# Kernel optimization log

Measured on AMD Instinct MI355X. Metric: run time of the kernel, lower is better.

## Reference

```python
import jax, jax.numpy as jnp
import numpy as np

UP = 2


def _lpf_rect(N, cutoff):
    # ideal lowpass rect over full-FFT frequency axis (with Nyquist 0.5 fix)
    cutoff_low = int((N * cutoff) // 2)
    cutoff_high = int(N - cutoff_low)
    rect = np.ones(N, dtype=np.float32)
    rect[cutoff_low + 1:cutoff_high] = 0.0
    if (N * cutoff) % 2 == 0:
        rect[cutoff_low] = 0.5
        rect[cutoff_high] = 0.5
    return rect


def _recon_rect(N, cutoff):
    # reconstruction rect for zero-insertion upsampling (no Nyquist halving)
    cutoff_low = int((N * cutoff) // 2)
    cutoff_high = int(N - cutoff_low)
    rect = np.ones(N, dtype=np.float32)
    rect[cutoff_low + 1:cutoff_high] = 0.0
    return rect


def _rfft2_mask(rect_h, rect_w):
    # outer product mask on rfft2 grid: full H axis x half W axis
    half_w = rect_w.shape[0] // 2 + 1
    return jnp.asarray(rect_h[:, None] * rect_w[None, :half_w])


def setup_inputs() -> dict:
    key = jax.random.key(0)
    x = jax.random.normal(key, (32, 128, 64, 64), dtype=jnp.float32)
    # PolyAct default init_coef (buffer, non-trainable)
    coef = jnp.array([0.0169394634313126, 0.5, 0.3078363963999393, 0.0],
                     dtype=jnp.float32)
    return {"x": x, "coef": coef}


def reference(x, coef):
    B, C, H, W = x.shape
    Hu, Wu = H * UP, W * UP

    # ---- UpsampleRFFT: zero-insertion then ideal reconstruction filter ----
    xu = jnp.zeros((B, C, Hu, Wu), x.dtype).at[:, :, ::UP, ::UP].set(x)
    recon_mask = _rfft2_mask(_recon_rect(Hu, 1.0 / UP), _recon_rect(Wu, 1.0 / UP))
    f = jnp.fft.rfft2(xu) * (UP * UP) * recon_mask
    xu = jnp.fft.irfft2(f, s=(Hu, Wu))

    # ---- PolyAct: calc_polynomial loops range(2, deg) with deg=3, so only
    # terms up to x^2 are used (coef[3] is never applied) ----
    y = coef[0] + coef[1] * xu + coef[2] * xu * xu

    # ---- LPF_RFFT with cutoff = 1/up ----
    lpf_mask = _rfft2_mask(_lpf_rect(Hu, 1.0 / UP), _lpf_rect(Wu, 1.0 / UP))
    y = jnp.fft.irfft2(jnp.fft.rfft2(y) * lpf_mask, s=(Hu, Wu))

    # ---- decimate back to original resolution ----
    return y[:, :, ::UP, ::UP]
```

## Files before the change

### kernel.cpp

```cpp
#include <hip/hip_runtime.h>
#include <math.h>


typedef short short8 __attribute__((ext_vector_type(8)));
typedef float f32x16 __attribute__((ext_vector_type(16)));

#define LSH 68

__device__ unsigned g_flag;
__device__ float g_gws[64];
__device__ __align__(16) short g_ftw[16 * 64 * 8];

__device__ __forceinline__ short f2bf(float f) {
  unsigned u = __float_as_uint(f);
  u += 0x7FFFu + ((u >> 16) & 1u);
  return (short)(u >> 16);
}
__device__ __forceinline__ float bf2f(short s) {
  return __uint_as_float(((unsigned)(unsigned short)s) << 16);
}
__device__ __forceinline__ short8 ldrow(const short* p) {
  union { unsigned u[4]; short8 s; } v;
  const uint2 lo = *(const uint2*)p;
  const uint2 hi = *(const uint2*)(p + 4);
  v.u[0] = lo.x; v.u[1] = lo.y; v.u[2] = hi.x; v.u[3] = hi.y;
  return v.s;
}
__device__ __forceinline__ unsigned pk2(short a, short b) {
  return (unsigned)(unsigned short)a | ((unsigned)(unsigned short)b << 16);
}

__global__ void uppolyact_setup() {
  if (g_flag == 0xC0FFEEu) return;
  __shared__ float g64s[64];
  const int tid = threadIdx.x;
  if (tid < 64) {
    const int d = 2 * tid + 1;
    float s = 1.0f;
    for (int k = 1; k <= 32; ++k) {
      const int qq = (k * d) & 127;
      s += 2.0f * cosf((float)M_PI * (1.0f / 64.0f) * (float)qq);
    }
    const float gv = s * (1.0f / 64.0f);
    g64s[tid] = gv;
    g_gws[tid] = gv;
  }
  __syncthreads();
#pragma unroll
  for (int e = 0; e < 4; ++e) {
    const int entry = tid + 256 * e;
    const int s_ = entry >> 6, ln = entry & 63;
    const int t_ = s_ >> 3, blk = (s_ >> 2) & 1, kk = s_ & 3;
    const int basei = kk * 16 + (ln >> 5) * 8 - (ln & 31) - 32 * blk;
    short* dst = &g_ftw[(s_ * 64 + ln) * 8];
#pragma unroll
    for (int j = 0; j < 8; ++j) {
      const int i0 = basei + j;
      const int idx = t_ ? ((-i0) & 63) : (i0 & 63);
      dst[j] = f2bf(g64s[idx]);
    }
  }
  __syncthreads();
  if (tid == 0) g_flag = 0xC0FFEEu;
}

__global__ __launch_bounds__(256, 4) void uppolyact_kernel(
    const float* __restrict__ x, const float* __restrict__ coef,
    float* __restrict__ out) {
  __shared__ __align__(16) short Xr[64 * LSH];
  __shared__ __align__(16) short XcZ[64 * LSH];
  __shared__ __align__(16) short LrU[64 * LSH];
  __shared__ __align__(16) short Zoo[64 * LSH];
  __shared__ float g64[64];
  __shared__ float tvec[64], uvec[64], sRv[64], Luv[64];
  __shared__ float sigv;

  const int tid = threadIdx.x;
  const int lane = tid & 63;
  const int w = tid >> 6;
  const int q = lane >> 5;
  const int l31 = lane & 31;
  const int rb = w >> 1, cb = w & 1;
  const int jcol = cb * 32 + l31;
  const size_t base = (size_t)blockIdx.x * 4096;
  const float* xb = x + base;
  const short8* ft8 = (const short8*)g_ftw;

  float xcur[16];
#pragma unroll
  for (int r = 0; r < 16; ++r) {
    const int irow = rb * 32 + (r & 3) + 4 * q + 8 * (r >> 2);
    xcur[r] = xb[irow * 64 + jcol];
  }

  short8 fA[4], fB[4];
#pragma unroll
  for (int kk = 0; kk < 4; ++kk) {
    fA[kk] = ft8[((2 + rb) * 4 + kk) * 64 + lane];
    fB[kk] = ft8[((2 + cb) * 4 + kk) * 64 + lane];
  }
  if (tid < 64) g64[tid] = g_gws[tid];

#pragma unroll
  for (int k = 0; k < 4; ++k) {
    const int irowb = rb * 32 + 4 * q + 8 * k;
    short b[4];
#pragma unroll
    for (int j = 0; j < 4; ++j) {
      b[j] = f2bf(xcur[4 * k + j]);
      Xr[(irowb + j) * LSH + jcol] = b[j];
    }
    uint2 p;
    p.x = pk2(b[0], b[1]);
    p.y = pk2(b[2], b[3]);
    *(uint2*)&XcZ[jcol * LSH + irowb] = p;
  }
  __syncthreads();

  {
    const int o = tid >> 1, h = tid & 1;
    const short* src = (o < 64) ? &XcZ[o * LSH + 32 * h]
                                : &Xr[(o - 64) * LSH + 32 * h];
    float acc = 0.0f;
#pragma unroll
    for (int p = 0; p < 4; ++p) {
      const short8 v = ldrow(src + 8 * p);
#pragma unroll
      for (int j = 0; j < 8; ++j) {
        const float f = bf2f(v[j]);
        acc += (j & 1) ? -f : f;
      }
    }
    acc += __shfl_xor(acc, 1);
    if (h == 0) {
      if (o < 64) tvec[o] = acc; else uvec[o - 64] = acc;
    }
  }
  __syncthreads();

  f32x16 Rt, Lt;
#pragma unroll
  for (int r = 0; r < 16; ++r) { Rt[r] = 0.0f; Lt[r] = 0.0f; }
#pragma unroll
  for (int kk = 0; kk < 4; ++kk) {
    const short8 bR = ldrow(&Xr[(cb * 32 + l31) * LSH + kk * 16 + q * 8]);
    Rt = __builtin_amdgcn_mfma_f32_32x32x16_bf16(fA[kk], bR, Rt, 0, 0, 0);
    const short8 aL = ldrow(&XcZ[(rb * 32 + l31) * LSH + kk * 16 + q * 8]);
    Lt = __builtin_amdgcn_mfma_f32_32x32x16_bf16(aL, fB[kk], Lt, 0, 0, 0);
  }
  {
    const int o = tid >> 1, h = tid & 1;
    const int o63 = o & 63;
    const float* vsrc = (o < 64) ? tvec : uvec;
    float acc = 0.0f;
#pragma unroll
    for (int p = 0; p < 32; ++p) {
      const int m = 32 * h + p;
      acc += vsrc[m] * g64[(o63 - m) & 63];
    }
    acc += __shfl_xor(acc, 1);
    if (h == 0) {
      if (o < 64) sRv[o] = acc; else Luv[o - 64] = acc;
    }
  }
  if (w == 0) {
    float sv = (lane & 1) ? -tvec[lane] : tvec[lane];
#pragma unroll
    for (int d_ = 1; d_ < 64; d_ <<= 1) sv += __shfl_xor(sv, d_);
    if (lane == 0) sigv = sv;
  }
  __syncthreads();

  float zoe[16];
  {
    const int icol = cb * 32 + l31;
    const float sgi = (icol & 1) ? -1.0f : 1.0f;
#pragma unroll
    for (int k = 0; k < 4; ++k) {
      const int jb = rb * 32 + 4 * q + 8 * k;
      short ze[4], zl[4];
#pragma unroll
      for (int t = 0; t < 4; ++t) {
        const int r = 4 * k + t;
        const int jrow = jb + t;
        const float sgj = (jrow & 1) ? -1.0f : 1.0f;
        const float veo = Rt[r] + sgi * sRv[jrow] * (1.0f / 64.0f);
        ze[t] = f2bf(veo * veo);
        zl[t] = f2bf(Lt[r]);
        const float voe = Lt[r] + Luv[icol] * sgj * (1.0f / 64.0f);
        zoe[r] = voe * voe;
      }
      uint2 pz, pl;
      pz.x = pk2(ze[0], ze[1]); pz.y = pk2(ze[2], ze[3]);
      pl.x = pk2(zl[0], zl[1]); pl.y = pk2(zl[2], zl[3]);
      *(uint2*)&XcZ[icol * LSH + jb] = pz;
      *(uint2*)&LrU[icol * LSH + jb] = pl;
    }
  }
  __syncthreads();

  short8 fU[4], fW[4];
#pragma unroll
  for (int kk = 0; kk < 4; ++kk) {
    fU[kk] = ft8[((0 + rb) * 4 + kk) * 64 + lane];
    fW[kk] = ft8[((0 + cb) * 4 + kk) * 64 + lane];
  }
  f32x16 OOt;
#pragma unroll
  for (int r = 0; r < 16; ++r) OOt[r] = 0.0f;
#pragma unroll
  for (int kk = 0; kk < 4; ++kk) {
    const short8 b = ldrow(&LrU[(cb * 32 + l31) * LSH + kk * 16 + q * 8]);
    OOt = __builtin_amdgcn_mfma_f32_32x32x16_bf16(fA[kk], b, OOt, 0, 0, 0);
  }
  {
    const int icol = cb * 32 + l31;
#pragma unroll
    for (int k = 0; k < 4; ++k) {
      const int jb = rb * 32 + 4 * q + 8 * k;
      short zo[4];
#pragma unroll
      for (int t = 0; t < 4; ++t) {
        const int r = 4 * k + t;
        zo[t] = f2bf(OOt[r] * OOt[r]);
      }
      uint2 p;
      p.x = pk2(zo[0], zo[1]); p.y = pk2(zo[2], zo[3]);
      *(uint2*)&Zoo[icol * LSH + jb] = p;
    }
  }
  __syncthreads();

  f32x16 Ut, Wv;
#pragma unroll
  for (int r = 0; r < 16; ++r) { Ut[r] = zoe[r]; Wv[r] = 0.0f; }
#pragma unroll
  for (int kk = 0; kk < 4; ++kk) {
    const short8 bU = ldrow(&Zoo[(cb * 32 + l31) * LSH + kk * 16 + q * 8]);
    Ut = __builtin_amdgcn_mfma_f32_32x32x16_bf16(fU[kk], bU, Ut, 0, 0, 0);
    const short8 aW = ldrow(&XcZ[(rb * 32 + l31) * LSH + kk * 16 + q * 8]);
    Wv = __builtin_amdgcn_mfma_f32_32x32x16_bf16(aW, fW[kk], Wv, 0, 0, 0);
  }
#pragma unroll
  for (int r = 0; r < 16; ++r) {
    const int jrow = rb * 32 + (r & 3) + 4 * q + 8 * (r >> 2);
    const int icol = cb * 32 + l31;
    LrU[jrow * LSH + icol] = f2bf(Ut[r]);
  }
  __syncthreads();

  f32x16 Vv;
#pragma unroll
  for (int r = 0; r < 16; ++r) Vv[r] = 0.0f;
#pragma unroll
  for (int kk = 0; kk < 4; ++kk) {
    const short8 b = ldrow(&LrU[(cb * 32 + l31) * LSH + kk * 16 + q * 8]);
    Vv = __builtin_amdgcn_mfma_f32_32x32x16_bf16(fU[kk], b, Vv, 0, 0, 0);
  }

  const float c0 = coef[0], c1 = coef[1];
  const float c2q = 0.25f * coef[2];
  float* ob = out + base;
#pragma unroll
  for (int r = 0; r < 16; ++r) {
    const int irow = rb * 32 + (r & 3) + 4 * q + 8 * (r >> 2);
    const float sgi = (irow & 1) ? -1.0f : 1.0f;
    const float sgj = (jcol & 1) ? -1.0f : 1.0f;
    const float xv_ = bf2f(f2bf(xcur[r]));
    const float vee = xv_ + (sgi * tvec[jcol] + uvec[irow] * sgj) * (1.0f / 64.0f) +
                      sgi * sgj * sigv * (1.0f / 4096.0f);
    const float zee = vee * vee;
    ob[irow * 64 + jcol] = c0 + c1 * xcur[r] + c2q * (zee + Vv[r] + Wv[r]);
  }
}

extern "C" void kernel_launch(void* const* d_in, const int* in_sizes, int n_in,
                              void* d_out, int out_size, void* d_ws,
                              size_t ws_size, hipStream_t stream) {
  const float* x = (const float*)d_in[0];
  const float* coef = (const float*)d_in[1];
  float* out = (float*)d_out;
  const int channels = out_size / 4096;
  uppolyact_setup<<<dim3(1), dim3(256), 0, stream>>>();
  uppolyact_kernel<<<dim3(channels), dim3(256), 0, stream>>>(x, coef, out);
}
```

Before: 126.5 us.

## Stage Fourier twiddle fragments in LDS instead of holding them in registers

The bf16 twiddle MFMA operands were held in 16 short8 registers per thread, loaded from global memory. They now go cooperatively into a shared ftab array, refilled once between phases, and each MFMA reads its fragment from LDS. The shared buffers are also reordered so one 64x68 tile is freed to hold the table. This lowers VGPR pressure and global fragment traffic, at the cost of extra LDS reads per MFMA and one more barrier.

```diff
diff --git a/kernel.cpp b/kernel.cpp
--- a/kernel.cpp
+++ b/kernel.cpp
@@ -4,6 +4,7 @@
 
 typedef short short8 __attribute__((ext_vector_type(8)));
 typedef float f32x16 __attribute__((ext_vector_type(16)));
+typedef float f32x4 __attribute__((ext_vector_type(4)));
 
 #define LSH 68
 
@@ -67,10 +68,10 @@
 __global__ __launch_bounds__(256, 4) void uppolyact_kernel(
     const float* __restrict__ x, const float* __restrict__ coef,
     float* __restrict__ out) {
-  __shared__ __align__(16) short Xr[64 * LSH];
-  __shared__ __align__(16) short XcZ[64 * LSH];
-  __shared__ __align__(16) short LrU[64 * LSH];
-  __shared__ __align__(16) short Zoo[64 * LSH];
+  __shared__ __align__(16) short bufA[64 * LSH];
+  __shared__ __align__(16) short bufB[64 * LSH];
+  __shared__ __align__(16) short bufC[64 * LSH];
+  __shared__ __align__(16) short ftab[8 * 64 * 8];
   __shared__ float g64[64];
   __shared__ float tvec[64], uvec[64], sRv[64], Luv[64];
   __shared__ float sigv;
@@ -84,7 +85,6 @@
   const int jcol = cb * 32 + l31;
   const size_t base = (size_t)blockIdx.x * 4096;
   const float* xb = x + base;
-  const short8* ft8 = (const short8*)g_ftw;
 
   float xcur[16];
 #pragma unroll
@@ -92,12 +92,11 @@
     const int irow = rb * 32 + (r & 3) + 4 * q + 8 * (r >> 2);
     xcur[r] = xb[irow * 64 + jcol];
   }
-
-  short8 fA[4], fB[4];
-#pragma unroll
-  for (int kk = 0; kk < 4; ++kk) {
-    fA[kk] = ft8[((2 + rb) * 4 + kk) * 64 + lane];
-    fB[kk] = ft8[((2 + cb) * 4 + kk) * 64 + lane];
+  f32x4 t0, t1;
+  {
+    const f32x4* fsrc = (const f32x4*)(g_ftw + 8 * 64 * 8);
+    t0 = fsrc[tid];
+    t1 = fsrc[tid + 256];
   }
   if (tid < 64) g64[tid] = g_gws[tid];
 
@@ -108,19 +107,24 @@
 #pragma unroll
     for (int j = 0; j < 4; ++j) {
       b[j] = f2bf(xcur[4 * k + j]);
-      Xr[(irowb + j) * LSH + jcol] = b[j];
+      bufA[(irowb + j) * LSH + jcol] = b[j];
     }
     uint2 p;
     p.x = pk2(b[0], b[1]);
     p.y = pk2(b[2], b[3]);
-    *(uint2*)&XcZ[jcol * LSH + irowb] = p;
+    *(uint2*)&bufB[jcol * LSH + irowb] = p;
+  }
+  {
+    f32x4* fdst = (f32x4*)ftab;
+    fdst[tid] = t0;
+    fdst[tid + 256] = t1;
   }
   __syncthreads();
 
   {
     const int o = tid >> 1, h = tid & 1;
-    const short* src = (o < 64) ? &XcZ[o * LSH + 32 * h]
-                                : &Xr[(o - 64) * LSH + 32 * h];
+    const short* src = (o < 64) ? &bufB[o * LSH + 32 * h]
+                                : &bufA[(o - 64) * LSH + 32 * h];
     float acc = 0.0f;
 #pragma unroll
     for (int p = 0; p < 4; ++p) {
@@ -143,10 +147,12 @@
   for (int r = 0; r < 16; ++r) { Rt[r] = 0.0f; Lt[r] = 0.0f; }
 #pragma unroll
   for (int kk = 0; kk < 4; ++kk) {
-    const short8 bR = ldrow(&Xr[(cb * 32 + l31) * LSH + kk * 16 + q * 8]);
-    Rt = __builtin_amdgcn_mfma_f32_32x32x16_bf16(fA[kk], bR, Rt, 0, 0, 0);
-    const short8 aL = ldrow(&XcZ[(rb * 32 + l31) * LSH + kk * 16 + q * 8]);
-    Lt = __builtin_amdgcn_mfma_f32_32x32x16_bf16(aL, fB[kk], Lt, 0, 0, 0);
+    const short8 aR = *(const short8*)&ftab[((rb * 4 + kk) * 64 + lane) * 8];
+    const short8 bR = ldrow(&bufA[(cb * 32 + l31) * LSH + kk * 16 + q * 8]);
+    Rt = __builtin_amdgcn_mfma_f32_32x32x16_bf16(aR, bR, Rt, 0, 0, 0);
+    const short8 aL = ldrow(&bufB[(rb * 32 + l31) * LSH + kk * 16 + q * 8]);
+    const short8 bL = *(const short8*)&ftab[((cb * 4 + kk) * 64 + lane) * 8];
+    Lt = __builtin_amdgcn_mfma_f32_32x32x16_bf16(aL, bL, Lt, 0, 0, 0);
   }
   {
     const int o = tid >> 1, h = tid & 1;
@@ -171,6 +177,12 @@
   }
   __syncthreads();
 
+  f32x4 u0, u1;
+  {
+    const f32x4* fsrc = (const f32x4*)g_ftw;
+    u0 = fsrc[tid];
+    u1 = fsrc[tid + 256];
+  }
   float zoe[16];
   {
     const int icol = cb * 32 + l31;
@@ -193,25 +205,20 @@
       uint2 pz, pl;
       pz.x = pk2(ze[0], ze[1]); pz.y = pk2(ze[2], ze[3]);
       pl.x = pk2(zl[0], zl[1]); pl.y = pk2(zl[2], zl[3]);
-      *(uint2*)&XcZ[icol * LSH + jb] = pz;
-      *(uint2*)&LrU[icol * LSH + jb] = pl;
-    }
-  }
-  __syncthreads();
-
-  short8 fU[4], fW[4];
+      *(uint2*)&bufA[icol * LSH + jb] = pz;
+      *(uint2*)&bufB[icol * LSH + jb] = pl;
+    }
+  }
+  __syncthreads();
+
+  f32x16 OOt;
+#pragma unroll
+  for (int r = 0; r < 16; ++r) OOt[r] = 0.0f;
 #pragma unroll
   for (int kk = 0; kk < 4; ++kk) {
-    fU[kk] = ft8[((0 + rb) * 4 + kk) * 64 + lane];
-    fW[kk] = ft8[((0 + cb) * 4 + kk) * 64 + lane];
-  }
-  f32x16 OOt;
-#pragma unroll
-  for (int r = 0; r < 16; ++r) OOt[r] = 0.0f;
-#pragma unroll
-  for (int kk = 0; kk < 4; ++kk) {
-    const short8 b = ldrow(&LrU[(cb * 32 + l31) * LSH + kk * 16 + q * 8]);
-    OOt = __builtin_amdgcn_mfma_f32_32x32x16_bf16(fA[kk], b, OOt, 0, 0, 0);
+    const short8 a = *(const short8*)&ftab[((rb * 4 + kk) * 64 + lane) * 8];
+    const short8 b = ldrow(&bufB[(cb * 32 + l31) * LSH + kk * 16 + q * 8]);
+    OOt = __builtin_amdgcn_mfma_f32_32x32x16_bf16(a, b, OOt, 0, 0, 0);
   }
   {
     const int icol = cb * 32 + l31;
@@ -226,8 +233,16 @@
       }
       uint2 p;
       p.x = pk2(zo[0], zo[1]); p.y = pk2(zo[2], zo[3]);
-      *(uint2*)&Zoo[icol * LSH + jb] = p;
-    }
+      *(uint2*)&bufC[icol * LSH + jb] = p;
+    }
+  }
+  asm volatile("" : "+v"(u0), "+v"(u1));
+  __syncthreads();
+
+  {
+    f32x4* fdst = (f32x4*)ftab;
+    fdst[tid] = u0;
+    fdst[tid + 256] = u1;
   }
   __syncthreads();
 
@@ -236,16 +251,18 @@
   for (int r = 0; r < 16; ++r) { Ut[r] = zoe[r]; Wv[r] = 0.0f; }
 #pragma unroll
   for (int kk = 0; kk < 4; ++kk) {
-    const short8 bU = ldrow(&Zoo[(cb * 32 + l31) * LSH + kk * 16 + q * 8]);
-    Ut = __builtin_amdgcn_mfma_f32_32x32x16_bf16(fU[kk], bU, Ut, 0, 0, 0);
-    const short8 aW = ldrow(&XcZ[(rb * 32 + l31) * LSH + kk * 16 + q * 8]);
-    Wv = __builtin_amdgcn_mfma_f32_32x32x16_bf16(aW, fW[kk], Wv, 0, 0, 0);
+    const short8 aU = *(const short8*)&ftab[((rb * 4 + kk) * 64 + lane) * 8];
+    const short8 bU = ldrow(&bufC[(cb * 32 + l31) * LSH + kk * 16 + q * 8]);
+    Ut = __builtin_amdgcn_mfma_f32_32x32x16_bf16(aU, bU, Ut, 0, 0, 0);
+    const short8 aW = ldrow(&bufA[(rb * 32 + l31) * LSH + kk * 16 + q * 8]);
+    const short8 bW = *(const short8*)&ftab[((cb * 4 + kk) * 64 + lane) * 8];
+    Wv = __builtin_amdgcn_mfma_f32_32x32x16_bf16(aW, bW, Wv, 0, 0, 0);
   }
 #pragma unroll
   for (int r = 0; r < 16; ++r) {
     const int jrow = rb * 32 + (r & 3) + 4 * q + 8 * (r >> 2);
     const int icol = cb * 32 + l31;
-    LrU[jrow * LSH + icol] = f2bf(Ut[r]);
+    bufB[jrow * LSH + icol] = f2bf(Ut[r]);
   }
   __syncthreads();
 
@@ -254,8 +271,9 @@
   for (int r = 0; r < 16; ++r) Vv[r] = 0.0f;
 #pragma unroll
   for (int kk = 0; kk < 4; ++kk) {
-    const short8 b = ldrow(&LrU[(cb * 32 + l31) * LSH + kk * 16 + q * 8]);
-    Vv = __builtin_amdgcn_mfma_f32_32x32x16_bf16(fU[kk], b, Vv, 0, 0, 0);
+    const short8 a = *(const short8*)&ftab[((rb * 4 + kk) * 64 + lane) * 8];
+    const short8 b = ldrow(&bufB[(cb * 32 + l31) * LSH + kk * 16 + q * 8]);
+    Vv = __builtin_amdgcn_mfma_f32_32x32x16_bf16(a, b, Vv, 0, 0, 0);
   }
 
   const float c0 = coef[0], c1 = coef[1];
```

Measured after the change: 127.7 us. No clear change (+1.0%).
